# Kernel optimization log

Hardware: AMD Instinct MI355X
Metric: run time of the kernel (lower is better)

The kernel has to match this reference:

```python
import jax, jax.numpy as jnp
import numpy as np
from jax import lax

D_MODEL = 256
D_INNER = 1024   # expand * d_model
D_STATE = 16
D_CONV = 4
DT_RANK = 16     # ceil(d_model / 16)
BATCH = 8
SEQ = 2048
EPS = 1e-05


def setup_inputs() -> dict:
    key = jax.random.key(0)
    ks = jax.random.split(key, 32)
    def nrm(k, shape, scale):
        return jax.random.normal(k, shape, jnp.float32) * scale
    inp = {"input": nrm(ks[0], (BATCH, SEQ, D_MODEL), 1.0)}
    for i, pre in enumerate(["fw", "bw"]):
        o = 1 + i * 8
        inp[pre + "_norm_w"] = jnp.ones((D_MODEL,), jnp.float32)
        inp[pre + "_in_proj"] = nrm(ks[o + 0], (2 * D_INNER, D_MODEL), D_MODEL ** -0.5)
        inp[pre + "_conv_w"] = nrm(ks[o + 1], (D_INNER, 1, D_CONV), D_CONV ** -0.5)
        inp[pre + "_conv_b"] = nrm(ks[o + 2], (D_INNER,), 0.1)
        inp[pre + "_x_proj"] = nrm(ks[o + 3], (DT_RANK + 2 * D_STATE, D_INNER), D_INNER ** -0.5)
        inp[pre + "_dt_w"] = nrm(ks[o + 4], (D_INNER, DT_RANK), DT_RANK ** -0.5)
        inp[pre + "_dt_b"] = nrm(ks[o + 5], (D_INNER,), 1.0) - 4.0  # softplus -> small dt, like mamba init
        inp[pre + "_A_log"] = jnp.log(jnp.tile(jnp.arange(1, D_STATE + 1, dtype=jnp.float32), (D_INNER, 1)))
        inp[pre + "_D"] = jnp.ones((D_INNER,), jnp.float32)
        inp[pre + "_out_proj"] = nrm(ks[o + 6], (D_MODEL, D_INNER), D_INNER ** -0.5)
    return inp


def _rmsnorm(x, w):
    return x * lax.rsqrt(jnp.mean(x * x, axis=-1, keepdims=True) + EPS) * w


def _mamba(x, in_proj, conv_w, conv_b, x_proj, dt_w, dt_b, A_log, Dp, out_proj):
    # x: [B, L, d_model]
    Bsz = x.shape[0]
    xz = jnp.einsum('bld,ed->ble', x, in_proj)          # [B, L, 2*D_INNER]
    xi, z = jnp.split(xz, 2, axis=-1)
    # depthwise causal conv over time, then SiLU
    xc = lax.conv_general_dilated(xi.transpose(0, 2, 1), conv_w, (1,), [(D_CONV - 1, 0)],
                                  feature_group_count=D_INNER,
                                  dimension_numbers=('NCH', 'OIH', 'NCH'))
    xc = jax.nn.silu(xc + conv_b[None, :, None]).transpose(0, 2, 1)  # [B, L, D_INNER]
    dbl = jnp.einsum('bld,ed->ble', xc, x_proj)          # [B, L, DT_RANK + 2*N]
    dt_low, Bm, Cm = jnp.split(dbl, [DT_RANK, DT_RANK + D_STATE], axis=-1)
    dt = jax.nn.softplus(jnp.einsum('blr,dr->bld', dt_low, dt_w) + dt_b)  # [B, L, D_INNER]
    A = -jnp.exp(A_log)                                   # [D_INNER, N]

    def step(h, t):
        u_t, dt_t, B_t, C_t = t                           # [B,Di], [B,Di], [B,N], [B,N]
        dA = jnp.exp(dt_t[:, :, None] * A)                # [B, Di, N]
        h = h * dA + (dt_t * u_t)[:, :, None] * B_t[:, None, :]
        y = jnp.einsum('bdn,bn->bd', h, C_t)
        return h, y

    h0 = jnp.zeros((Bsz, D_INNER, D_STATE), x.dtype)
    xs = (xc.transpose(1, 0, 2), dt.transpose(1, 0, 2), Bm.transpose(1, 0, 2), Cm.transpose(1, 0, 2))
    _, ys = lax.scan(step, h0, xs)                        # ys: [L, B, Di]
    y = ys.transpose(1, 0, 2) + xc * Dp
    y = y * jax.nn.silu(z)
    return jnp.einsum('bld,ed->ble', y, out_proj)         # [B, L, d_model]


def _block(x, p):
    # Block with fused_add_norm=False, mlp=Identity, n_layer=1:
    # residual = x; h = mixer(rmsnorm(residual)); return h + residual
    h = _mamba(_rmsnorm(x, p[0]), *p[1:])
    return h + x


def reference(input, fw_norm_w, fw_in_proj, fw_conv_w, fw_conv_b, fw_x_proj, fw_dt_w, fw_dt_b,
              fw_A_log, fw_D, fw_out_proj, bw_norm_w, bw_in_proj, bw_conv_w, bw_conv_b, bw_x_proj,
              bw_dt_w, bw_dt_b, bw_A_log, bw_D, bw_out_proj):
    fwd = _block(input, (fw_norm_w, fw_in_proj, fw_conv_w, fw_conv_b, fw_x_proj, fw_dt_w,
                         fw_dt_b, fw_A_log, fw_D, fw_out_proj))
    bwd = _block(jnp.flip(input, 1), (bw_norm_w, bw_in_proj, bw_conv_w, bw_conv_b, bw_x_proj,
                                      bw_dt_w, bw_dt_b, bw_A_log, bw_D, bw_out_proj))
    bwd = jnp.flip(bwd, 1)
    return jnp.concatenate([fwd, bwd], axis=-1)           # [B, L, 2*d_model]
```

## Files before the change

### kernel.cpp

```cpp
#include <hip/hip_runtime.h>

typedef unsigned short u16;
typedef __bf16 bf16x8 __attribute__((ext_vector_type(8)));
typedef float f32x4 __attribute__((ext_vector_type(4)));

#define D_MODEL 256
#define D_INNER 1024
#define NST     16
#define SEQ     2048
#define LOG2E   1.4426950408889634f

struct TrueT  { static constexpr bool value = true;  };
struct FalseT { static constexpr bool value = false; };

static __device__ __forceinline__ float bf2f(u16 u) {
    union { float f; unsigned v; } x; x.v = ((unsigned)u) << 16; return x.f;
}
static __device__ __forceinline__ u16 f2bf(float f) {
    union { float f; unsigned u; } x; x.f = f;
    unsigned r = 0x7FFF + ((x.u >> 16) & 1);
    return (u16)((x.u + r) >> 16);
}

#define GLOAD_LDS16(g, l)                                            \
    __builtin_amdgcn_global_load_lds(                                \
        (const __attribute__((address_space(1))) void*)(g),          \
        (__attribute__((address_space(3))) void*)(l), 16, 0, 0)

static __device__ __forceinline__ void dA_pow(float e1, float* dA) {
    float e2 = e1 * e1, e3 = e2 * e1, e4 = e2 * e2;
    float e8 = e4 * e4, e12 = e8 * e4;
    dA[0] = e1;       dA[1] = e2;       dA[2] = e3;       dA[3] = e4;
    dA[4] = e4 * e1;  dA[5] = e4 * e2;  dA[6] = e4 * e3;  dA[7] = e8;
    dA[8] = e8 * e1;  dA[9] = e8 * e2;  dA[10] = e8 * e3; dA[11] = e12;
    dA[12] = e12 * e1; dA[13] = e12 * e2; dA[14] = e12 * e3; dA[15] = e8 * e8;
}

__global__ __launch_bounds__(256) void rmsnorm_k(const float* __restrict__ x,
                                                 const float* __restrict__ w,
                                                 u16* __restrict__ xnp) {
    int row = blockIdx.x, t = threadIdx.x;
    float v = x[(size_t)row * D_MODEL + t];
    float s = v * v;
    #pragma unroll
    for (int o = 32; o; o >>= 1) s += __shfl_xor(s, o, 64);
    __shared__ float red[4];
    if ((t & 63) == 0) red[t >> 6] = s;
    __syncthreads();
    float tot = red[0] + red[1] + red[2] + red[3];
    float scale = rsqrtf(tot * (1.0f / D_MODEL) + 1e-5f);
    float xv = v * scale * w[t];
    u16 hi = f2bf(xv);
    u16 lo = f2bf(xv - bf2f(hi));
    xnp[(size_t)row * 512 + t] = hi;
    xnp[(size_t)row * 512 + 256 + t] = lo;
}

__global__ __launch_bounds__(256) void wsplit_k(const float* __restrict__ src,
                                                u16* __restrict__ dst, int K) {
    int i = blockIdx.x * 256 + threadIdx.x;
    int n = i / K, k = i - n * K;
    float v = src[i];
    u16 hi = f2bf(v);
    u16 lo = f2bf(v - bf2f(hi));
    dst[(size_t)n * 2 * K + k] = hi;
    dst[(size_t)n * 2 * K + K + k] = lo;
}

__global__ __launch_bounds__(256) void wsplit_pad_k(const float* __restrict__ src,
                                                    u16* __restrict__ dst, int K,
                                                    int Nreal) {
    int i = blockIdx.x * 256 + threadIdx.x;
    int n = i / K, k = i - n * K;
    float v = 0.0f;
    if (n < Nreal) v = src[i];
    u16 hi = f2bf(v);
    u16 lo = f2bf(v - bf2f(hi));
    dst[(size_t)n * 2 * K + k] = hi;
    dst[(size_t)n * 2 * K + K + k] = lo;
}

__global__ __launch_bounds__(256) void gemm_mfma(const u16* __restrict__ Ap, int lda,
                                                 const u16* __restrict__ Wp, int ldw,
                                                 float* __restrict__ C, int ldc,
                                                 int KL, int kslice, size_t zstride,
                                                 int Nreal) {
    __shared__ u16 As[128][64];
    __shared__ u16 Ws[128][64];
    const int m0 = blockIdx.x * 128, n0 = blockIdx.y * 128;
    const int tid = threadIdx.x;
    const int wave = tid >> 6, lane = tid & 63;
    const int wm = (wave >> 1) * 64, wn = (wave & 1) * 64;
    const int lm = lane & 15, quad = lane >> 4;

    const int srow = lane >> 3;
    const int schunk = (lane & 7) ^ srow;
    const int rloc = wave * 8 + srow;

    f32x4 acc[4][4] = {};

    const int kb0 = blockIdx.z * kslice;
    for (int k0 = kb0; k0 < kb0 + kslice; k0 += 64) {
        int t = k0 / KL;
        int ko = k0 - t * KL;
        int ka = ko + (t == 2 ? KL : 0) + schunk * 8;
        int kw = ko + (t == 1 ? KL : 0) + schunk * 8;
        #pragma unroll
        for (int p = 0; p < 4; p++) {
            int row = p * 32 + rloc;
            GLOAD_LDS16(Ap + (size_t)(m0 + row) * lda + ka,
                        &As[p * 32 + wave * 8][0]);
            GLOAD_LDS16(Wp + (size_t)(n0 + row) * ldw + kw,
                        &Ws[p * 32 + wave * 8][0]);
        }
        __syncthreads();
        const int sc = lm & 7;
        #pragma unroll
        for (int kk = 0; kk < 2; kk++) {
            const int ch = ((kk << 2) | quad) ^ sc;
            bf16x8 af[4], bv[4];
            #pragma unroll
            for (int i = 0; i < 4; i++)
                af[i] = *(const bf16x8*)&As[wm + i * 16 + lm][ch * 8];
            #pragma unroll
            for (int j = 0; j < 4; j++)
                bv[j] = *(const bf16x8*)&Ws[wn + j * 16 + lm][ch * 8];
            #pragma unroll
            for (int i = 0; i < 4; i++)
                #pragma unroll
                for (int j = 0; j < 4; j++)
                    acc[i][j] = __builtin_amdgcn_mfma_f32_16x16x32_bf16(
                        af[i], bv[j], acc[i][j], 0, 0, 0);
        }
        __syncthreads();
    }

    float* Cz = C + zstride * blockIdx.z;
    #pragma unroll
    for (int i = 0; i < 4; i++)
        #pragma unroll
        for (int j = 0; j < 4; j++)
            #pragma unroll
            for (int r = 0; r < 4; r++) {
                int mrow = m0 + wm + i * 16 + quad * 4 + r;
                int ncol = n0 + wn + j * 16 + lm;
                if (ncol < Nreal)
                    Cz[(size_t)mrow * ldc + ncol] = acc[i][j][r];
            }
}

__global__ __launch_bounds__(256) void reduce_dbl_k(const float* __restrict__ pbuf,
                                                    float* __restrict__ dbl,
                                                    size_t RS) {
    size_t e = (size_t)blockIdx.x * 256 + threadIdx.x;
    float v = 0.0f;
    #pragma unroll
    for (int z = 0; z < 8; z++) v += pbuf[z * RS + e];
    dbl[e] = v;
}

__global__ __launch_bounds__(256) void reduce_out_k(const float* __restrict__ pbuf,
                                                    const float* __restrict__ res,
                                                    float* __restrict__ out,
                                                    int M, int coff) {
    int idx = blockIdx.x * 256 + threadIdx.x;
    int m = idx >> 6, n4 = (idx & 63) * 4;
    size_t e = (size_t)m * 256 + n4;
    size_t stride = (size_t)M * 256;
    float4 v = *(const float4*)(res + e);
    #pragma unroll
    for (int s = 0; s < 4; s++) {
        float4 p = *(const float4*)(pbuf + s * stride + e);
        v.x += p.x; v.y += p.y; v.z += p.z; v.w += p.w;
    }
    *(float4*)(out + (size_t)m * 512 + coff + n4) = v;
}

__global__ __launch_bounds__(256) void conv_silu_k(const float* __restrict__ xz,
                                                   const float* __restrict__ cw,
                                                   const float* __restrict__ cb,
                                                   u16* __restrict__ xcp, int dir) {
    int bx = blockIdx.x;
    int dgrp = bx & 3;
    int rowgrp = bx >> 2;
    int l0 = (rowgrp & (SEQ / 4 - 1)) * 4;
    int b = rowgrp >> 9;
    int d = dgrp * 256 + threadIdx.x;

    int base = dir ? l0 : (l0 - 3);
    float x[7];
    #pragma unroll
    for (int i = 0; i < 7; i++) {
        int lr = base + i;
        x[i] = (lr >= 0 && lr < SEQ)
             ? xz[((size_t)b * SEQ + lr) * (2 * D_INNER) + d] : 0.0f;
    }
    float w0 = cw[d * 4 + 0], w1 = cw[d * 4 + 1];
    float w2 = cw[d * 4 + 2], w3 = cw[d * 4 + 3];
    float bias = cb[d];

    #pragma unroll
    for (int li = 0; li < 4; li++) {
        float acc;
        if (dir == 0)
            acc = bias + w0 * x[li] + w1 * x[li + 1] + w2 * x[li + 2] + w3 * x[li + 3];
        else
            acc = bias + w3 * x[li] + w2 * x[li + 1] + w1 * x[li + 2] + w0 * x[li + 3];
        float s = acc / (1.0f + __expf(-acc));
        u16 hi = f2bf(s);
        u16 lo = f2bf(s - bf2f(hi));
        size_t row = (size_t)b * SEQ + l0 + li;
        xcp[row * 2048 + d] = hi;
        xcp[row * 2048 + D_INNER + d] = lo;
    }
}

__global__ __launch_bounds__(256) void scan_p1(const u16* __restrict__ xcp,
                                               const float* __restrict__ dbl,
                                               const float* __restrict__ dtw,
                                               const float* __restrict__ dtb,
                                               const float* __restrict__ Alog,
                                               float* __restrict__ P,
                                               float* __restrict__ H,
                                               int nb, int TC, int dir) {
    __shared__ float sdbl[32 * 48];
    int t = threadIdx.x;
    int nblk4 = nb * 4;
    int c = blockIdx.x / nblk4;
    int rem = blockIdx.x - c * nblk4;
    int b = rem >> 2, dblk = rem & 3;
    int d = dblk * 256 + t;

    int lbase = dir ? (SEQ - (c + 1) * TC) : (c * TC);
    {
        const float* src = dbl + ((size_t)b * SEQ + lbase) * 48;
        int nf4 = TC * 12;
        for (int i = t; i < nf4; i += 256)
            *(float4*)&sdbl[i * 4] = *(const float4*)(src + i * 4);
    }

    float A2[16], wdt[16];
    const float* ap = Alog + (size_t)d * NST;
    const float* wp = dtw + (size_t)d * NST;
    #pragma unroll
    for (int n = 0; n < 16; n++) { A2[n] = -__expf(ap[n]) * LOG2E; wdt[n] = wp[n]; }
    float bdt = dtb[d];
    bool fast = true;
    #pragma unroll
    for (int n = 0; n < 16; n++)
        fast = fast && (fabsf(A2[n] - (n + 1) * A2[0]) < 1e-3f);

    float h[16] = {0,0,0,0,0,0,0,0,0,0,0,0,0,0,0,0};
    float S = 0.0f;

    int lstep = dir ? -1 : 1;
    int l0 = dir ? (lbase + TC - 1) : lbase;
    const u16* up = xcp + ((size_t)b * SEQ + l0) * 2048 + d;
    ptrdiff_t ups = (ptrdiff_t)lstep * 2048;
    const float* dr = sdbl + (dir ? (TC - 1) * 48 : 0);
    ptrdiff_t drs = (ptrdiff_t)lstep * 48;

    __syncthreads();

    auto body = [&](auto FC) {
        constexpr bool F = decltype(FC)::value;
        #pragma unroll 2
        for (int s = 0; s < TC; s++) {
            float dl[16], B[16];
            #pragma unroll
            for (int n = 0; n < 16; n += 4) {
                *(float4*)&dl[n] = *(const float4*)(dr + n);
                *(float4*)&B[n]  = *(const float4*)(dr + 16 + n);
            }
            float u = bf2f(up[0]) + bf2f(up[D_INNER]);
            float acc = bdt;
            #pragma unroll
            for (int n = 0; n < 16; n++) acc += dl[n] * wdt[n];
            float dt = (acc > 20.0f) ? acc : __logf(1.0f + __expf(acc));
            float dtu = dt * u;
            S += dt;
            float dA[16];
            if (F) {
                dA_pow(exp2f(A2[0] * dt), dA);
            } else {
                #pragma unroll
                for (int n = 0; n < 16; n++) dA[n] = exp2f(A2[n] * dt);
            }
            #pragma unroll
            for (int n = 0; n < 16; n++)
                h[n] = h[n] * dA[n] + dtu * B[n];
            dr += drs; up += ups;
        }
    };
    if (fast) body(TrueT{}); else body(FalseT{});

    size_t NCH = (size_t)nb * 16384;
    size_t base = (size_t)c * NCH + ((size_t)b * 1024 + d) * 16;
    float Pv[16];
    if (fast) {
        dA_pow(exp2f(A2[0] * S), Pv);
    } else {
        #pragma unroll
        for (int n = 0; n < 16; n++) Pv[n] = exp2f(A2[n] * S);
    }
    #pragma unroll
    for (int n = 0; n < 16; n += 4) {
        *(float4*)&H[base + n] = *(float4*)&h[n];
        *(float4*)&P[base + n] = *(float4*)&Pv[n];
    }
}

__global__ __launch_bounds__(256) void scan_p2(const float* __restrict__ P,
                                               float* __restrict__ H,
                                               int NCH, int NC) {
    size_t chain = (size_t)blockIdx.x * 256 + threadIdx.x;
    float h = 0.0f;
    for (int c = 0; c < NC; c++) {
        size_t i = (size_t)c * NCH + chain;
        float Hc = H[i], Pc = P[i];
        H[i] = h;
        h = Hc + Pc * h;
    }
}

__global__ __launch_bounds__(256) void scan_p3(const u16* __restrict__ xcp,
                                               const float* __restrict__ dbl,
                                               const float* __restrict__ dtw,
                                               const float* __restrict__ dtb,
                                               float* __restrict__ xz,
                                               const float* __restrict__ Alog,
                                               const float* __restrict__ Dp,
                                               const float* __restrict__ hin,
                                               int nb, int TC, int dir) {
    __shared__ float sdbl[32 * 48];
    int t = threadIdx.x;
    int nblk4 = nb * 4;
    int c = blockIdx.x / nblk4;
    int rem = blockIdx.x - c * nblk4;
    int b = rem >> 2, dblk = rem & 3;
    int d = dblk * 256 + t;

    int lbase = dir ? (SEQ - (c + 1) * TC) : (c * TC);
    {
        const float* src = dbl + ((size_t)b * SEQ + lbase) * 48;
        int nf4 = TC * 12;
        for (int i = t; i < nf4; i += 256)
            *(float4*)&sdbl[i * 4] = *(const float4*)(src + i * 4);
    }

    float A2[16], wdt[16];
    const float* ap = Alog + (size_t)d * NST;
    const float* wp = dtw + (size_t)d * NST;
    #pragma unroll
    for (int n = 0; n < 16; n++) { A2[n] = -__expf(ap[n]) * LOG2E; wdt[n] = wp[n]; }
    float bdt = dtb[d];
    float Dd = Dp[d];
    bool fast = true;
    #pragma unroll
    for (int n = 0; n < 16; n++)
        fast = fast && (fabsf(A2[n] - (n + 1) * A2[0]) < 1e-3f);

    size_t NCH = (size_t)nb * 16384;
    size_t base = (size_t)c * NCH + ((size_t)b * 1024 + d) * 16;
    float h[16];
    #pragma unroll
    for (int n = 0; n < 16; n += 4)
        *(float4*)&h[n] = *(const float4*)&hin[base + n];

    int lstep = dir ? -1 : 1;
    int l0 = dir ? (lbase + TC - 1) : lbase;
    size_t row0 = (size_t)b * SEQ + l0;
    const u16* up = xcp + row0 * 2048 + d;
    const float* zp = xz + row0 * 2048 + D_INNER + d;
    u16* yp = (u16*)(xz + row0 * 2048) + d;
    ptrdiff_t ups = (ptrdiff_t)lstep * 2048;
    ptrdiff_t zps = (ptrdiff_t)lstep * 2048;
    ptrdiff_t yps = (ptrdiff_t)lstep * 4096;
    const float* dr = sdbl + (dir ? (TC - 1) * 48 : 0);
    ptrdiff_t drs = (ptrdiff_t)lstep * 48;

    __syncthreads();

    auto body = [&](auto FC) {
        constexpr bool F = decltype(FC)::value;
        #pragma unroll 2
        for (int s = 0; s < TC; s++) {
            float dl[16], B[16], Cv[16];
            #pragma unroll
            for (int n = 0; n < 16; n += 4) {
                *(float4*)&dl[n] = *(const float4*)(dr + n);
                *(float4*)&B[n]  = *(const float4*)(dr + 16 + n);
                *(float4*)&Cv[n] = *(const float4*)(dr + 32 + n);
            }
            float u = bf2f(up[0]) + bf2f(up[D_INNER]);
            float acc = bdt;
            #pragma unroll
            for (int n = 0; n < 16; n++) acc += dl[n] * wdt[n];
            float dt = (acc > 20.0f) ? acc : __logf(1.0f + __expf(acc));
            float dtu = dt * u;
            float dA[16];
            if (F) {
                dA_pow(exp2f(A2[0] * dt), dA);
            } else {
                #pragma unroll
                for (int n = 0; n < 16; n++) dA[n] = exp2f(A2[n] * dt);
            }
            #pragma unroll
            for (int n = 0; n < 16; n++)
                h[n] = h[n] * dA[n] + dtu * B[n];

            float p0 = h[0]*Cv[0] + h[1]*Cv[1] + h[2]*Cv[2] + h[3]*Cv[3];
            float p1 = h[4]*Cv[4] + h[5]*Cv[5] + h[6]*Cv[6] + h[7]*Cv[7];
            float p2 = h[8]*Cv[8] + h[9]*Cv[9] + h[10]*Cv[10] + h[11]*Cv[11];
            float p3 = h[12]*Cv[12] + h[13]*Cv[13] + h[14]*Cv[14] + h[15]*Cv[15];

            float z = *zp;
            float g = z / (1.0f + __expf(-z));
            float y = ((p0 + p1) + (p2 + p3) + u * Dd) * g;

            u16 hi = f2bf(y);
            yp[0] = hi;
            yp[D_INNER] = f2bf(y - bf2f(hi));

            dr += drs; up += ups; zp += zps; yp += yps;
        }
    };
    if (fast) body(TrueT{}); else body(FalseT{});
}

extern "C" void kernel_launch(void* const* d_in, const int* in_sizes, int n_in,
                              void* d_out, int out_size, void* d_ws, size_t ws_size,
                              hipStream_t stream) {
    const float* input = (const float*)d_in[0];
    float* out = (float*)d_out;

    const size_t phfix = (size_t)2 * 256 * 16384 * 4;
    const size_t perb  = (size_t)2048 * (256 + 2048 + 1024 + 48) * 4;
    const size_t wspl  = (size_t)(2048 * 512 + 256 * 2048 + 128 * 2048) * 2;
    int nb = 4;
    while (nb > 1 && phfix + (size_t)nb * perb + wspl > ws_size) nb >>= 1;
    const int NC = 256 / nb;
    const int TC = SEQ / NC;
    const int R = nb * SEQ;
    const int NCH = nb * 16384;

    float* P    = (float*)d_ws;
    float* H    = P + (size_t)256 * 16384;
    float* xnf  = H + (size_t)256 * 16384;
    float* xz   = xnf + (size_t)R * D_MODEL;
    float* xcyf = xz  + (size_t)R * 2 * D_INNER;
    float* dbl  = xcyf + (size_t)R * D_INNER;
    u16*  winp  = (u16*)(dbl + (size_t)R * 48);
    u16*  woutp = winp + (size_t)2048 * 512;
    u16*  xpp   = woutp + (size_t)256 * 2048;
    u16*  xnp   = (u16*)xnf;
    u16*  xcp   = (u16*)xcyf;

    for (int dir = 0; dir < 2; dir++) {
        int o = 1 + dir * 10;
        const float* nw   = (const float*)d_in[o + 0];
        const float* win  = (const float*)d_in[o + 1];
        const float* cw   = (const float*)d_in[o + 2];
        const float* cb   = (const float*)d_in[o + 3];
        const float* xp   = (const float*)d_in[o + 4];
        const float* dtw  = (const float*)d_in[o + 5];
        const float* dtbv = (const float*)d_in[o + 6];
        const float* Alog = (const float*)d_in[o + 7];
        const float* Dp   = (const float*)d_in[o + 8];
        const float* wout = (const float*)d_in[o + 9];

        wsplit_k<<<2048 * 256 / 256, 256, 0, stream>>>(win, winp, D_MODEL);
        wsplit_k<<<256 * 1024 / 256, 256, 0, stream>>>(wout, woutp, D_INNER);
        wsplit_pad_k<<<128 * 1024 / 256, 256, 0, stream>>>(xp, xpp, D_INNER, 48);

        for (int b0 = 0; b0 < 8; b0 += nb) {
            const float* xin = input + (size_t)b0 * SEQ * D_MODEL;
            float* cout = out + (size_t)b0 * SEQ * 2 * D_MODEL;

            rmsnorm_k<<<R, 256, 0, stream>>>(xin, nw, xnp);
            gemm_mfma<<<dim3(R / 128, 16, 1), 256, 0, stream>>>(
                xnp, 512, winp, 512, xz, 2 * D_INNER, D_MODEL, 3 * D_MODEL, 0,
                2 * D_INNER);
            conv_silu_k<<<R, 256, 0, stream>>>(xz, cw, cb, xcp, dir);
            gemm_mfma<<<dim3(R / 128, 1, 8), 256, 0, stream>>>(
                xcp, 2048, xpp, 2048, P, 48, D_INNER, 384, (size_t)R * 48, 48);
            reduce_dbl_k<<<R * 48 / 256, 256, 0, stream>>>(P, dbl, (size_t)R * 48);
            scan_p1<<<NC * nb * 4, 256, 0, stream>>>(
                xcp, dbl, dtw, dtbv, Alog, P, H, nb, TC, dir);
            scan_p2<<<NCH / 256, 256, 0, stream>>>(P, H, NCH, NC);
            scan_p3<<<NC * nb * 4, 256, 0, stream>>>(
                xcp, dbl, dtw, dtbv, xz, Alog, Dp, H, nb, TC, dir);
            gemm_mfma<<<dim3(R / 128, 2, 4), 256, 0, stream>>>(
                (const u16*)xz, 4096, woutp, 2048, P, 256, D_INNER, 768,
                (size_t)R * 256, 256);
            reduce_out_k<<<R * 64 / 256, 256, 0, stream>>>(
                P, xin, cout, R, dir * D_MODEL);
        }
    }
}
```

Before: 885.5 us.

## Add 256x256-tile triple-buffered MFMA GEMM for in_proj and out_proj

Introduces a new GEMM kernel with 512 threads and 256x256 output tiles. It uses a three-stage LDS ring filled by direct global-to-LDS loads, XOR-swizzled LDS reads, and raised wave priority around the MFMA bursts. The in_proj and out_proj GEMMs switch to this kernel to get more data reuse per tile and to overlap loads with compute. The cost is a larger LDS footprint, more accumulator registers per thread, and fewer blocks on the grid, which can hurt occupancy and load balance across CUs.

```diff
diff --git a/kernel.cpp b/kernel.cpp
--- a/kernel.cpp
+++ b/kernel.cpp
@@ -138,6 +138,135 @@
     float* Cz = C + zstride * blockIdx.z;
     #pragma unroll
     for (int i = 0; i < 4; i++)
+        #pragma unroll
+        for (int j = 0; j < 4; j++)
+            #pragma unroll
+            for (int r = 0; r < 4; r++) {
+                int mrow = m0 + wm + i * 16 + quad * 4 + r;
+                int ncol = n0 + wn + j * 16 + lm;
+                if (ncol < Nreal)
+                    Cz[(size_t)mrow * ldc + ncol] = acc[i][j][r];
+            }
+}
+
+__global__ __launch_bounds__(512, 2) void gemm_mfma2(const u16* __restrict__ Ap, int lda,
+                                                     const u16* __restrict__ Wp, int ldw,
+                                                     float* __restrict__ C, int ldc,
+                                                     int KL, int kslice, size_t zstride,
+                                                     int Nreal) {
+    __shared__ u16 As[3][256][32];
+    __shared__ u16 Ws[3][256][32];
+    const int m0 = blockIdx.x * 256, n0 = blockIdx.y * 256;
+    const int tid = threadIdx.x;
+    const int wave = tid >> 6, lane = tid & 63;
+    const int wm = (wave >> 2) * 128, wn = (wave & 3) * 64;
+    const int lm = lane & 15, quad = lane >> 4;
+
+    const int srow = lane >> 2;
+    const int schunk = (lane & 3) ^ (srow & 3);
+    const int KL2 = 2 * KL;
+
+    const int NT = kslice / 32;
+    const int kb0 = blockIdx.z * kslice;
+
+    const u16* Arow = Ap + (size_t)(m0 + wave * 16 + srow) * lda + schunk * 8;
+    const u16* Wrow = Wp + (size_t)(n0 + wave * 16 + srow) * ldw + schunk * 8;
+    const size_t ldA = (size_t)128 * lda;
+    const size_t ldW = (size_t)128 * ldw;
+    u16* AsW = &As[0][wave * 16][0];
+    u16* WsW = &Ws[0][wave * 16][0];
+
+    f32x4 acc[8][4] = {};
+
+    auto koffs = [&](int ts, int& ka, int& kw) {
+        int ks = kb0 + ts * 32;
+        int t = (ks >= KL2) ? 2 : (ks >= KL ? 1 : 0);
+        int ko = ks - t * KL;
+        ka = ko + (t == 2 ? KL : 0);
+        kw = ko + (t == 1 ? KL : 0);
+    };
+
+    {
+        int ka, kw;
+        koffs(0, ka, kw);
+        GLOAD_LDS16(Arow + ka, AsW);
+        GLOAD_LDS16(Arow + ldA + ka, AsW + 4096);
+        GLOAD_LDS16(Wrow + kw, WsW);
+        GLOAD_LDS16(Wrow + ldW + kw, WsW + 4096);
+        koffs(1, ka, kw);
+        GLOAD_LDS16(Arow + ka, AsW + 8192);
+        GLOAD_LDS16(Arow + ldA + ka, AsW + 8192 + 4096);
+        GLOAD_LDS16(Wrow + kw, WsW + 8192);
+        GLOAD_LDS16(Wrow + ldW + kw, WsW + 8192 + 4096);
+    }
+    asm volatile("s_waitcnt vmcnt(4)" ::: "memory");
+    __syncthreads();
+
+    int cur = 0, stg = 2;
+    const int rdsw = (quad ^ (lm & 3)) * 8;
+    for (int tt = 0; tt < NT; ++tt) {
+        const u16* Ab = &As[cur][0][0];
+        const u16* Wb = &Ws[cur][0][0];
+        const bool pre = (tt + 2 < NT);
+        int ka = 0, kw = 0;
+        if (pre) koffs(tt + 2, ka, kw);
+
+        bf16x8 bv[4], af[4];
+        #pragma unroll
+        for (int j = 0; j < 4; j++) {
+            int r = wn + j * 16 + lm;
+            bv[j] = *(const bf16x8*)(Wb + r * 32 + ((quad ^ (r & 3)) * 8));
+        }
+        #pragma unroll
+        for (int i = 0; i < 4; i++) {
+            int r = wm + i * 16 + lm;
+            af[i] = *(const bf16x8*)(Ab + r * 32 + ((quad ^ (r & 3)) * 8));
+        }
+        if (pre) {
+            GLOAD_LDS16(Arow + ka, AsW + stg * 8192);
+            GLOAD_LDS16(Arow + ldA + ka, AsW + stg * 8192 + 4096);
+        }
+        __syncthreads();
+        __builtin_amdgcn_s_setprio(1);
+        #pragma unroll
+        for (int i = 0; i < 4; i++)
+            #pragma unroll
+            for (int j = 0; j < 4; j++)
+                acc[i][j] = __builtin_amdgcn_mfma_f32_16x16x32_bf16(
+                    af[i], bv[j], acc[i][j], 0, 0, 0);
+        __builtin_amdgcn_s_setprio(0);
+        __syncthreads();
+
+        #pragma unroll
+        for (int i = 0; i < 4; i++) {
+            int r = wm + 64 + i * 16 + lm;
+            af[i] = *(const bf16x8*)(Ab + r * 32 + ((quad ^ (r & 3)) * 8));
+        }
+        if (pre) {
+            GLOAD_LDS16(Wrow + kw, WsW + stg * 8192);
+            GLOAD_LDS16(Wrow + ldW + kw, WsW + stg * 8192 + 4096);
+        }
+        __syncthreads();
+        __builtin_amdgcn_s_setprio(1);
+        #pragma unroll
+        for (int i = 0; i < 4; i++)
+            #pragma unroll
+            for (int j = 0; j < 4; j++)
+                acc[4 + i][j] = __builtin_amdgcn_mfma_f32_16x16x32_bf16(
+                    af[i], bv[j], acc[4 + i][j], 0, 0, 0);
+        __builtin_amdgcn_s_setprio(0);
+        if (pre) asm volatile("s_waitcnt vmcnt(4)" ::: "memory");
+        else     asm volatile("s_waitcnt vmcnt(0)" ::: "memory");
+        __syncthreads();
+
+        cur = (cur == 2) ? 0 : cur + 1;
+        stg = (stg == 2) ? 0 : stg + 1;
+    }
+    (void)rdsw;
+
+    float* Cz = C + zstride * blockIdx.z;
+    #pragma unroll
+    for (int i = 0; i < 8; i++)
         #pragma unroll
         for (int j = 0; j < 4; j++)
             #pragma unroll
@@ -478,7 +607,7 @@
             float* cout = out + (size_t)b0 * SEQ * 2 * D_MODEL;
 
             rmsnorm_k<<<R, 256, 0, stream>>>(xin, nw, xnp);
-            gemm_mfma<<<dim3(R / 128, 16, 1), 256, 0, stream>>>(
+            gemm_mfma2<<<dim3(R / 256, 8, 1), 512, 0, stream>>>(
                 xnp, 512, winp, 512, xz, 2 * D_INNER, D_MODEL, 3 * D_MODEL, 0,
                 2 * D_INNER);
             conv_silu_k<<<R, 256, 0, stream>>>(xz, cw, cb, xcp, dir);
@@ -490,7 +619,7 @@
             scan_p2<<<NCH / 256, 256, 0, stream>>>(P, H, NCH, NC);
             scan_p3<<<NC * nb * 4, 256, 0, stream>>>(
                 xcp, dbl, dtw, dtbv, xz, Alog, Dp, H, nb, TC, dir);
-            gemm_mfma<<<dim3(R / 128, 2, 4), 256, 0, stream>>>(
+            gemm_mfma2<<<dim3(R / 256, 1, 4), 512, 0, stream>>>(
                 (const u16*)xz, 4096, woutp, 2048, P, 256, D_INNER, 768,
                 (size_t)R * 256, 256);
             reduce_out_k<<<R * 64 / 256, 256, 0, stream>>>(
```

Result: slower. 992.3 us (+12.1%).

## Load hi/lo bf16 split once per K-step and issue three MFMAs per tile

Applied to the files above, without the earlier changes.

The split-bf16 GEMM used to walk the K axis three times, once per hi*hi, hi*lo and lo*hi term, reloading operands on each pass. Now each LDS tile holds 32 hi and 32 lo columns from the same K range, and all three products are issued from a single load. This cuts global and LDS traffic for the A and W tiles by about a third. Separately, the scan kernels prefetch the next step's u and z values one iteration ahead to hide load latency. Both changes add register pressure.

```diff
diff --git a/kernel.cpp b/kernel.cpp
--- a/kernel.cpp
+++ b/kernel.cpp
@@ -95,42 +95,44 @@
 
     const int srow = lane >> 3;
     const int schunk = (lane & 7) ^ srow;
+    const int scol = (schunk < 4) ? schunk * 8 : KL + (schunk - 4) * 8;
     const int rloc = wave * 8 + srow;
 
     f32x4 acc[4][4] = {};
 
     const int kb0 = blockIdx.z * kslice;
-    for (int k0 = kb0; k0 < kb0 + kslice; k0 += 64) {
-        int t = k0 / KL;
-        int ko = k0 - t * KL;
-        int ka = ko + (t == 2 ? KL : 0) + schunk * 8;
-        int kw = ko + (t == 1 ? KL : 0) + schunk * 8;
+    for (int ko = kb0; ko < kb0 + kslice; ko += 32) {
         #pragma unroll
         for (int p = 0; p < 4; p++) {
             int row = p * 32 + rloc;
-            GLOAD_LDS16(Ap + (size_t)(m0 + row) * lda + ka,
+            GLOAD_LDS16(Ap + (size_t)(m0 + row) * lda + ko + scol,
                         &As[p * 32 + wave * 8][0]);
-            GLOAD_LDS16(Wp + (size_t)(n0 + row) * ldw + kw,
+            GLOAD_LDS16(Wp + (size_t)(n0 + row) * ldw + ko + scol,
                         &Ws[p * 32 + wave * 8][0]);
         }
         __syncthreads();
-        const int sc = lm & 7;
+        const int ph = ((quad ^ lm) & 7) * 8;
+        bf16x8 bh[4], bl[4];
         #pragma unroll
-        for (int kk = 0; kk < 2; kk++) {
-            const int ch = ((kk << 2) | quad) ^ sc;
-            bf16x8 af[4], bv[4];
-            #pragma unroll
-            for (int i = 0; i < 4; i++)
-                af[i] = *(const bf16x8*)&As[wm + i * 16 + lm][ch * 8];
-            #pragma unroll
-            for (int j = 0; j < 4; j++)
-                bv[j] = *(const bf16x8*)&Ws[wn + j * 16 + lm][ch * 8];
-            #pragma unroll
-            for (int i = 0; i < 4; i++)
-                #pragma unroll
-                for (int j = 0; j < 4; j++)
-                    acc[i][j] = __builtin_amdgcn_mfma_f32_16x16x32_bf16(
-                        af[i], bv[j], acc[i][j], 0, 0, 0);
+        for (int j = 0; j < 4; j++) {
+            const u16* wr = &Ws[wn + j * 16 + lm][0];
+            bh[j] = *(const bf16x8*)(wr + ph);
+            bl[j] = *(const bf16x8*)(wr + (ph ^ 32));
+        }
+        #pragma unroll
+        for (int i = 0; i < 4; i++) {
+            const u16* ar = &As[wm + i * 16 + lm][0];
+            bf16x8 ah = *(const bf16x8*)(ar + ph);
+            bf16x8 al = *(const bf16x8*)(ar + (ph ^ 32));
+            #pragma unroll
+            for (int j = 0; j < 4; j++) {
+                acc[i][j] = __builtin_amdgcn_mfma_f32_16x16x32_bf16(
+                    ah, bh[j], acc[i][j], 0, 0, 0);
+                acc[i][j] = __builtin_amdgcn_mfma_f32_16x16x32_bf16(
+                    ah, bl[j], acc[i][j], 0, 0, 0);
+                acc[i][j] = __builtin_amdgcn_mfma_f32_16x16x32_bf16(
+                    al, bh[j], acc[i][j], 0, 0, 0);
+            }
         }
         __syncthreads();
     }
@@ -264,15 +266,17 @@
 
     auto body = [&](auto FC) {
         constexpr bool F = decltype(FC)::value;
+        u16 uh = up[0], ul = up[D_INNER];
         #pragma unroll 2
         for (int s = 0; s < TC; s++) {
+            u16 nh = up[ups], nl = up[ups + D_INNER];
             float dl[16], B[16];
             #pragma unroll
             for (int n = 0; n < 16; n += 4) {
                 *(float4*)&dl[n] = *(const float4*)(dr + n);
                 *(float4*)&B[n]  = *(const float4*)(dr + 16 + n);
             }
-            float u = bf2f(up[0]) + bf2f(up[D_INNER]);
+            float u = bf2f(uh) + bf2f(ul);
             float acc = bdt;
             #pragma unroll
             for (int n = 0; n < 16; n++) acc += dl[n] * wdt[n];
@@ -289,6 +293,7 @@
             #pragma unroll
             for (int n = 0; n < 16; n++)
                 h[n] = h[n] * dA[n] + dtu * B[n];
+            uh = nh; ul = nl;
             dr += drs; up += ups;
         }
     };
@@ -383,8 +388,12 @@
 
     auto body = [&](auto FC) {
         constexpr bool F = decltype(FC)::value;
+        u16 uh = up[0], ul = up[D_INNER];
+        float zc = *zp;
         #pragma unroll 2
         for (int s = 0; s < TC; s++) {
+            u16 nh = up[ups], nl = up[ups + D_INNER];
+            float zn = zp[zps];
             float dl[16], B[16], Cv[16];
             #pragma unroll
             for (int n = 0; n < 16; n += 4) {
@@ -392,7 +401,7 @@
                 *(float4*)&B[n]  = *(const float4*)(dr + 16 + n);
                 *(float4*)&Cv[n] = *(const float4*)(dr + 32 + n);
             }
-            float u = bf2f(up[0]) + bf2f(up[D_INNER]);
+            float u = bf2f(uh) + bf2f(ul);
             float acc = bdt;
             #pragma unroll
             for (int n = 0; n < 16; n++) acc += dl[n] * wdt[n];
@@ -414,14 +423,14 @@
             float p2 = h[8]*Cv[8] + h[9]*Cv[9] + h[10]*Cv[10] + h[11]*Cv[11];
             float p3 = h[12]*Cv[12] + h[13]*Cv[13] + h[14]*Cv[14] + h[15]*Cv[15];
 
-            float z = *zp;
-            float g = z / (1.0f + __expf(-z));
+            float g = zc / (1.0f + __expf(-zc));
             float y = ((p0 + p1) + (p2 + p3) + u * Dd) * g;
 
             u16 hi = f2bf(y);
             yp[0] = hi;
             yp[D_INNER] = f2bf(y - bf2f(hi));
 
+            uh = nh; ul = nl; zc = zn;
             dr += drs; up += ups; zp += zps; yp += yps;
         }
     };
@@ -479,11 +488,12 @@
 
             rmsnorm_k<<<R, 256, 0, stream>>>(xin, nw, xnp);
             gemm_mfma<<<dim3(R / 128, 16, 1), 256, 0, stream>>>(
-                xnp, 512, winp, 512, xz, 2 * D_INNER, D_MODEL, 3 * D_MODEL, 0,
+                xnp, 512, winp, 512, xz, 2 * D_INNER, D_MODEL, D_MODEL, 0,
                 2 * D_INNER);
             conv_silu_k<<<R, 256, 0, stream>>>(xz, cw, cb, xcp, dir);
             gemm_mfma<<<dim3(R / 128, 1, 8), 256, 0, stream>>>(
-                xcp, 2048, xpp, 2048, P, 48, D_INNER, 384, (size_t)R * 48, 48);
+                xcp, 2048, xpp, 2048, P, 48, D_INNER, D_INNER / 8,
+                (size_t)R * 48, 48);
             reduce_dbl_k<<<R * 48 / 256, 256, 0, stream>>>(P, dbl, (size_t)R * 48);
             scan_p1<<<NC * nb * 4, 256, 0, stream>>>(
                 xcp, dbl, dtw, dtbv, Alog, P, H, nb, TC, dir);
@@ -491,7 +501,7 @@
             scan_p3<<<NC * nb * 4, 256, 0, stream>>>(
                 xcp, dbl, dtw, dtbv, xz, Alog, Dp, H, nb, TC, dir);
             gemm_mfma<<<dim3(R / 128, 2, 4), 256, 0, stream>>>(
-                (const u16*)xz, 4096, woutp, 2048, P, 256, D_INNER, 768,
+                (const u16*)xz, 4096, woutp, 2048, P, 256, D_INNER, D_INNER / 4,
                 (size_t)R * 256, 256);
             reduce_out_k<<<R * 64 / 256, 256, 0, stream>>>(
                 P, xin, cout, R, dir * D_MODEL);
```

After: 864.0 us. 2.4% less time.
